# Kernel optimization log

Measured on AMD Instinct MI355X. Metric: run time of the kernel, lower is better.

## Reference

```python
import jax, jax.numpy as jnp
import numpy as np
import math

B, S, H, NH = 2, 2048, 2048, 16
HD = H // NH  # 128


def _rope_tables(seq_len, dim, base=10000.0):
    inv_freq = 1.0 / (base ** (np.arange(0, dim, 2, dtype=np.float32) / dim))
    t = np.arange(seq_len, dtype=np.float32)
    freqs = np.outer(t, inv_freq)                      # [S, dim/2]
    emb = np.concatenate([freqs, freqs], axis=-1)      # [S, dim] (HF layout)
    return jnp.asarray(np.cos(emb)), jnp.asarray(np.sin(emb))


def setup_inputs() -> dict:
    key = jax.random.key(0)
    ks = jax.random.split(key, 6)
    sc = 1.0 / math.sqrt(H)
    cos, sin = _rope_tables(S, HD)
    return {
        "hidden_states": jax.random.normal(ks[0], (B, S, H), jnp.float32),
        "wq": jax.random.normal(ks[1], (H, H), jnp.float32) * sc,
        "wk": jax.random.normal(ks[2], (H, H), jnp.float32) * sc,
        "wv": jax.random.normal(ks[3], (H, H), jnp.float32) * sc,
        "wo": jax.random.normal(ks[4], (H, H), jnp.float32) * sc,
        "cos": cos,
        "sin": sin,
        "attention_mask": jnp.ones((B, S), jnp.float32),
        "position_ids": jnp.broadcast_to(jnp.arange(S, dtype=jnp.int64), (B, S)),
    }


def _rotate_half(x):
    x1, x2 = jnp.split(x, 2, axis=-1)
    return jnp.concatenate([-x2, x1], axis=-1)


def reference(hidden_states, wq, wk, wv, wo, cos, sin, attention_mask, position_ids):
    b, s, _ = hidden_states.shape
    # projections (torch Linear: x @ W^T)
    q = (hidden_states @ wq.T).reshape(b, s, NH, HD).transpose(0, 2, 1, 3)
    k = (hidden_states @ wk.T).reshape(b, s, NH, HD).transpose(0, 2, 1, 3)
    v = (hidden_states @ wv.T).reshape(b, s, NH, HD).transpose(0, 2, 1, 3)
    # RoPE (HF apply_rotary_pos_emb): gather tables at position_ids -> [b,1,s,hd]
    c = cos[position_ids][:, None, :, :]
    sn = sin[position_ids][:, None, :, :]
    q = q * c + _rotate_half(q) * sn
    k = k * c + _rotate_half(k) * sn
    # dense attention scores [b,h,q,k]
    scores = jnp.einsum("bhqd,bhkd->bhqk", q, k) / math.sqrt(HD)
    adder = (1.0 - attention_mask)[:, None, None, :] * -10000.0
    scores = scores + adder
    probs = jax.nn.softmax(scores.astype(jnp.float32), axis=-1).astype(q.dtype)
    attn = jnp.einsum("bhqk,bhkd->bhqd", probs, v)
    attn = attn.transpose(0, 2, 1, 3).reshape(b, s, H)
    return attn @ wo.T
```

## Files before the change

### kernel.cpp

```cpp
#include <hip/hip_runtime.h>
#include <hip/hip_bf16.h>

#define B_SZ 2
#define S_LEN 2048
#define H_DIM 2048
#define N_HEAD 16
#define HD 128

using bf16 = __hip_bfloat16;
using bf16x8 = __bf16 __attribute__((ext_vector_type(8)));
using floatx4 = float __attribute__((ext_vector_type(4)));

typedef unsigned int __attribute__((address_space(1))) as1_uint;
typedef unsigned int __attribute__((address_space(3))) as3_uint;

__device__ inline void async_load16(const void* g, void* l) {
  __builtin_amdgcn_global_load_lds((const as1_uint*)g, (as3_uint*)l, 16, 0, 0);
}

__device__ inline void store_out(float* p, float v) { *p = v; }
__device__ inline void store_out(bf16* p, float v) { *p = __float2bfloat16(v); }

__global__ __launch_bounds__(256) void cast_kernel(const float* __restrict__ in,
                                                   bf16* __restrict__ out, int n4) {
  int i = blockIdx.x * 256 + threadIdx.x;
  if (i >= n4) return;
  const float4 v = ((const float4*)in)[i];
  union { bf16 h[4]; uint2 u; } o;
  o.h[0] = __float2bfloat16(v.x);
  o.h[1] = __float2bfloat16(v.y);
  o.h[2] = __float2bfloat16(v.z);
  o.h[3] = __float2bfloat16(v.w);
  ((uint2*)out)[i] = o.u;
}

__global__ __launch_bounds__(256) void cast4_kernel(
    const float* __restrict__ a, const float* __restrict__ b,
    const float* __restrict__ c, const float* __restrict__ d,
    bf16* __restrict__ oa, bf16* __restrict__ ob,
    bf16* __restrict__ oc, bf16* __restrict__ od) {
  int i = blockIdx.x * 256 + threadIdx.x;
  int sel = i >> 20;
  int j = i & 0xFFFFF;
  const float* src = sel == 0 ? a : sel == 1 ? b : sel == 2 ? c : d;
  bf16* dst = sel == 0 ? oa : sel == 1 ? ob : sel == 2 ? oc : od;
  const float4 v = ((const float4*)src)[j];
  union { bf16 h[4]; uint2 u; } o;
  o.h[0] = __float2bfloat16(v.x);
  o.h[1] = __float2bfloat16(v.y);
  o.h[2] = __float2bfloat16(v.z);
  o.h[3] = __float2bfloat16(v.w);
  ((uint2*)dst)[j] = o.u;
}

template <typename OutT>
__global__ __launch_bounds__(256) void gemm_bt(const bf16* __restrict__ A,
                                               const bf16* __restrict__ B,
                                               OutT* __restrict__ C,
                                               int M, int N, int K) {
  __shared__ alignas(16) bf16 As[128 * 32];
  __shared__ alignas(16) bf16 Bs[128 * 32];
  const int tid = threadIdx.x;
  const int wave = tid >> 6;
  const int lane = tid & 63;
  const int quad = lane >> 4;
  const int l16 = lane & 15;
  const int m0 = blockIdx.x * 128;
  const int n0 = blockIdx.y * 128;
  const int wm = (wave >> 1) * 64;
  const int wn = (wave & 1) * 64;

  const bf16* Ag = A + (size_t)(m0 + (tid >> 2)) * K + (tid & 3) * 8;
  const bf16* Bg = B + (size_t)(n0 + (tid >> 2)) * K + (tid & 3) * 8;
  char* AsB = (char*)As + wave * 1024;
  char* BsB = (char*)Bs + wave * 1024;
  const size_t rowskip = (size_t)64 * K;

  floatx4 acc[4][4] = {};

  for (int k0 = 0; k0 < K; k0 += 32) {
    async_load16(Ag + k0, AsB);
    async_load16(Ag + rowskip + k0, AsB + 4096);
    async_load16(Bg + k0, BsB);
    async_load16(Bg + rowskip + k0, BsB + 4096);
    __syncthreads();

    bf16x8 af[4], bfr[4];
#pragma unroll
    for (int i = 0; i < 4; i++)
      af[i] = *(const bf16x8*)&As[(wm + i * 16 + l16) * 32 + quad * 8];
#pragma unroll
    for (int j = 0; j < 4; j++)
      bfr[j] = *(const bf16x8*)&Bs[(wn + j * 16 + l16) * 32 + quad * 8];
#pragma unroll
    for (int i = 0; i < 4; i++)
#pragma unroll
      for (int j = 0; j < 4; j++)
        acc[i][j] = __builtin_amdgcn_mfma_f32_16x16x32_bf16(af[i], bfr[j], acc[i][j], 0, 0, 0);
    __syncthreads();
  }

#pragma unroll
  for (int i = 0; i < 4; i++) {
    const int row = m0 + wm + i * 16 + quad * 4;
#pragma unroll
    for (int j = 0; j < 4; j++) {
      const int col = n0 + wn + j * 16 + l16;
#pragma unroll
      for (int r = 0; r < 4; r++)
        store_out(&C[(size_t)(row + r) * N + col], acc[i][j][r]);
    }
  }
}

__global__ __launch_bounds__(256) void gemm_qk_rope(
    const bf16* __restrict__ A, const bf16* __restrict__ B, bf16* __restrict__ C,
    const float* __restrict__ cosT, const float* __restrict__ sinT,
    const int* __restrict__ pos, int K) {
  __shared__ alignas(16) bf16 As[128 * 32];
  __shared__ alignas(16) bf16 Bs[128 * 32];
  const int tid = threadIdx.x;
  const int wave = tid >> 6;
  const int lane = tid & 63;
  const int quad = lane >> 4;
  const int l16 = lane & 15;
  const int m0 = blockIdx.x * 128;
  const int n0 = blockIdx.y * 128;
  const int wm = wave * 32;

  const bf16* Ag = A + (size_t)(m0 + (tid >> 2)) * K + (tid & 3) * 8;
  const bf16* Bg = B + (size_t)(n0 + (tid >> 2)) * K + (tid & 3) * 8;
  char* AsB = (char*)As + wave * 1024;
  char* BsB = (char*)Bs + wave * 1024;
  const size_t rowskip = (size_t)64 * K;

  floatx4 acc[2][8] = {};

  for (int k0 = 0; k0 < K; k0 += 32) {
    async_load16(Ag + k0, AsB);
    async_load16(Ag + rowskip + k0, AsB + 4096);
    async_load16(Bg + k0, BsB);
    async_load16(Bg + rowskip + k0, BsB + 4096);
    __syncthreads();

    bf16x8 af[2], bfr[8];
#pragma unroll
    for (int i = 0; i < 2; i++)
      af[i] = *(const bf16x8*)&As[(wm + i * 16 + l16) * 32 + quad * 8];
#pragma unroll
    for (int j = 0; j < 8; j++)
      bfr[j] = *(const bf16x8*)&Bs[(j * 16 + l16) * 32 + quad * 8];
#pragma unroll
    for (int i = 0; i < 2; i++)
#pragma unroll
      for (int j = 0; j < 8; j++)
        acc[i][j] = __builtin_amdgcn_mfma_f32_16x16x32_bf16(af[i], bfr[j], acc[i][j], 0, 0, 0);
    __syncthreads();
  }

  const float sc = (n0 < 2048) ? 0.08838834764831845f : 1.0f;
#pragma unroll
  for (int i = 0; i < 2; i++) {
    const int row0 = m0 + wm + i * 16 + quad * 4;
#pragma unroll
    for (int r = 0; r < 4; r++) {
      const int row = row0 + r;
      const int p = pos[row];
      const float* cp = cosT + (size_t)p * HD;
      const float* sp = sinT + (size_t)p * HD;
      bf16* Crow = C + (size_t)row * 4096 + n0 + l16;
#pragma unroll
      for (int j = 0; j < 4; j++) {
        const int d = j * 16 + l16;
        const float c = cp[d], s = sp[d];
        const float v1 = acc[i][j][r], v2 = acc[i][j + 4][r];
        Crow[j * 16] = __float2bfloat16((v1 * c - v2 * s) * sc);
        Crow[j * 16 + 64] = __float2bfloat16((v2 * c + v1 * s) * sc);
      }
    }
  }
}

__global__ __launch_bounds__(256, 2) void flash_attn(
    const bf16* __restrict__ QK, const bf16* __restrict__ Vt,
    const float* __restrict__ mask, bf16* __restrict__ AO) {
  __shared__ alignas(16) bf16 KP[128 * 136];
  __shared__ alignas(16) bf16 Vs[128 * 136];
  const int tid = threadIdx.x;
  const int wave = tid >> 6;
  const int lane = tid & 63;
  const int quad = lane >> 4;
  const int l16 = lane & 15;
  const int b = blockIdx.x >> 4;
  const int h = blockIdx.x & 15;
  const int q0 = blockIdx.y * 128;

  const bf16* Qb = QK + (size_t)(b * S_LEN + q0) * 4096 + h * HD;
  const bf16* Kb = QK + (size_t)(b * S_LEN) * 4096 + 2048 + h * HD;
  const bf16* Vb = Vt + (size_t)(h * HD) * 4096 + (size_t)b * S_LEN;
  const float* Mb = mask + b * S_LEN;

  bf16x8 qf[2][4];
#pragma unroll
  for (int s = 0; s < 2; s++)
#pragma unroll
    for (int kc = 0; kc < 4; kc++)
      qf[s][kc] = *(const bf16x8*)(Qb + (size_t)(wave * 32 + s * 16 + l16) * 4096 +
                                   kc * 32 + quad * 8);

  float l_i[2][4] = {};
  floatx4 O[2][8] = {};

  for (int k0 = 0; k0 < S_LEN; k0 += 128) {
    for (int i = tid; i < 2048; i += 256) {
      int r = i >> 4;
      int c = (i & 15) * 8;
      *(uint4*)&KP[r * 136 + c] = *(const uint4*)(Kb + (size_t)(k0 + r) * 4096 + c);
      *(uint4*)&Vs[r * 136 + c] = *(const uint4*)(Vb + (size_t)r * 4096 + k0 + c);
    }
    __syncthreads();

    floatx4 Sa[2][8] = {};
#pragma unroll
    for (int ct = 0; ct < 8; ct++) {
      bf16x8 kf[4];
#pragma unroll
      for (int kc = 0; kc < 4; kc++)
        kf[kc] = *(const bf16x8*)&KP[(ct * 16 + l16) * 136 + kc * 32 + quad * 8];
#pragma unroll
      for (int s = 0; s < 2; s++)
#pragma unroll
        for (int kc = 0; kc < 4; kc++)
          Sa[s][ct] = __builtin_amdgcn_mfma_f32_16x16x32_bf16(qf[s][kc], kf[kc], Sa[s][ct], 0, 0, 0);
    }
    __syncthreads();

    float addv[8];
#pragma unroll
    for (int ct = 0; ct < 8; ct++)
      addv[ct] = (1.0f - Mb[k0 + ct * 16 + l16]) * -10000.0f - 12.0f;

#pragma unroll
    for (int s = 0; s < 2; s++) {
      const int qrow = (wave * 32 + s * 16 + quad * 4) * 136;
#pragma unroll
      for (int ct = 0; ct < 8; ct++)
#pragma unroll
        for (int r = 0; r < 4; r++) {
          float p = __expf(Sa[s][ct][r] + addv[ct]);
          l_i[s][r] += p;
          KP[qrow + r * 136 + ct * 16 + l16] = __float2bfloat16(p);
        }
    }

#pragma unroll
    for (int kc = 0; kc < 4; kc++) {
      bf16x8 pa[2];
#pragma unroll
      for (int s = 0; s < 2; s++)
        pa[s] = *(const bf16x8*)&KP[(wave * 32 + s * 16 + l16) * 136 + kc * 32 + quad * 8];
#pragma unroll
      for (int dt = 0; dt < 8; dt++) {
        bf16x8 vf = *(const bf16x8*)&Vs[(dt * 16 + l16) * 136 + kc * 32 + quad * 8];
#pragma unroll
        for (int s = 0; s < 2; s++)
          O[s][dt] = __builtin_amdgcn_mfma_f32_16x16x32_bf16(pa[s], vf, O[s][dt], 0, 0, 0);
      }
    }
    __syncthreads();
  }

#pragma unroll
  for (int s = 0; s < 2; s++)
#pragma unroll
    for (int r = 0; r < 4; r++)
#pragma unroll
      for (int off = 1; off < 16; off <<= 1)
        l_i[s][r] += __shfl_xor(l_i[s][r], off);

#pragma unroll
  for (int s = 0; s < 2; s++) {
    const int qrow = q0 + wave * 32 + s * 16 + quad * 4;
#pragma unroll
    for (int r = 0; r < 4; r++) {
      float inv = 1.0f / l_i[s][r];
      bf16* outp = AO + (size_t)(b * S_LEN + qrow + r) * H_DIM + h * HD + l16;
#pragma unroll
      for (int dt = 0; dt < 8; dt++)
        outp[dt * 16] = __float2bfloat16(O[s][dt][r] * inv);
    }
  }
}

extern "C" void kernel_launch(void* const* d_in, const int* in_sizes, int n_in,
                              void* d_out, int out_size, void* d_ws, size_t ws_size,
                              hipStream_t stream) {
  const float* hs   = (const float*)d_in[0];
  const float* wq   = (const float*)d_in[1];
  const float* wk   = (const float*)d_in[2];
  const float* wv   = (const float*)d_in[3];
  const float* wo   = (const float*)d_in[4];
  const float* cosT = (const float*)d_in[5];
  const float* sinT = (const float*)d_in[6];
  const float* mask = (const float*)d_in[7];
  const int*   pos  = (const int*)d_in[8];

  char* ws = (char*)d_ws;
  bf16* Xbf  = (bf16*)ws;
  bf16* Wqkb = (bf16*)(ws + (size_t)(16 << 20));
  bf16* Wvb  = (bf16*)(ws + (size_t)(32 << 20));
  bf16* Wob  = (bf16*)(ws + (size_t)(40 << 20));
  bf16* QKm  = (bf16*)(ws + (size_t)(48 << 20));
  bf16* Vtm  = (bf16*)(ws + (size_t)(80 << 20));
  bf16* AO   = Xbf;

  cast_kernel<<<8192, 256, 0, stream>>>(hs, Xbf, 2097152);
  cast4_kernel<<<16384, 256, 0, stream>>>(wq, wk, wv, wo,
                                          Wqkb, Wqkb + (size_t)2048 * 2048, Wvb, Wob);

  gemm_qk_rope<<<dim3(32, 32), 256, 0, stream>>>(Xbf, Wqkb, QKm, cosT, sinT, pos, 2048);
  gemm_bt<bf16><<<dim3(16, 32), 256, 0, stream>>>(Wvb, Xbf, Vtm, 2048, 4096, 2048);

  flash_attn<<<dim3(32, 16), 256, 0, stream>>>(QKm, Vtm, mask, AO);

  gemm_bt<float><<<dim3(32, 16), 256, 0, stream>>>(AO, Wob, (float*)d_out, 4096, 2048, 2048);
}
```

Measured before the change: 460.9 us.

## Rewrite QK+RoPE GEMM with 256x256 tiles and double-buffered swizzled LDS pipeline

```diff
diff --git a/kernel.cpp b/kernel.cpp
--- a/kernel.cpp
+++ b/kernel.cpp
@@ -113,64 +113,123 @@
   }
 }
 
-__global__ __launch_bounds__(256) void gemm_qk_rope(
-    const bf16* __restrict__ A, const bf16* __restrict__ B, bf16* __restrict__ C,
-    const float* __restrict__ cosT, const float* __restrict__ sinT,
-    const int* __restrict__ pos, int K) {
-  __shared__ alignas(16) bf16 As[128 * 32];
-  __shared__ alignas(16) bf16 Bs[128 * 32];
+__global__ __launch_bounds__(512, 2) void gemm_qk_rope256(
+    const bf16* __restrict__ A, const bf16* __restrict__ B,
+    bf16* __restrict__ C, const float* __restrict__ cosT,
+    const float* __restrict__ sinT, const int* __restrict__ pos) {
+  __shared__ alignas(16) char lds[131072];
   const int tid = threadIdx.x;
-  const int wave = tid >> 6;
+  const int wv = tid >> 6;
   const int lane = tid & 63;
   const int quad = lane >> 4;
   const int l16 = lane & 15;
-  const int m0 = blockIdx.x * 128;
-  const int n0 = blockIdx.y * 128;
-  const int wm = wave * 32;
-
-  const bf16* Ag = A + (size_t)(m0 + (tid >> 2)) * K + (tid & 3) * 8;
-  const bf16* Bg = B + (size_t)(n0 + (tid >> 2)) * K + (tid & 3) * 8;
-  char* AsB = (char*)As + wave * 1024;
-  char* BsB = (char*)Bs + wave * 1024;
-  const size_t rowskip = (size_t)64 * K;
-
-  floatx4 acc[2][8] = {};
-
-  for (int k0 = 0; k0 < K; k0 += 32) {
-    async_load16(Ag + k0, AsB);
-    async_load16(Ag + rowskip + k0, AsB + 4096);
-    async_load16(Bg + k0, BsB);
-    async_load16(Bg + rowskip + k0, BsB + 4096);
-    __syncthreads();
-
-    bf16x8 af[2], bfr[8];
-#pragma unroll
-    for (int i = 0; i < 2; i++)
-      af[i] = *(const bf16x8*)&As[(wm + i * 16 + l16) * 32 + quad * 8];
-#pragma unroll
-    for (int j = 0; j < 8; j++)
-      bfr[j] = *(const bf16x8*)&Bs[(j * 16 + l16) * 32 + quad * 8];
-#pragma unroll
-    for (int i = 0; i < 2; i++)
-#pragma unroll
-      for (int j = 0; j < 8; j++)
-        acc[i][j] = __builtin_amdgcn_mfma_f32_16x16x32_bf16(af[i], bfr[j], acc[i][j], 0, 0, 0);
-    __syncthreads();
-  }
-
-  const float sc = (n0 < 2048) ? 0.08838834764831845f : 1.0f;
-#pragma unroll
-  for (int i = 0; i < 2; i++) {
-    const int row0 = m0 + wm + i * 16 + quad * 4;
-#pragma unroll
-    for (int r = 0; r < 4; r++) {
-      const int row = row0 + r;
+  const int lrow = lane >> 3;
+  const int scol = ((lane & 7) << 4) ^ (lrow << 4);
+
+  const int id = blockIdx.x;
+  const int swz = (id & 7) * 32 + (id >> 3);
+  const int m0 = (swz >> 4) * 256;
+  const int n0 = (swz & 15) * 256;
+  const int wrow = (wv >> 1) * 64;
+  const int wcol = (wv & 1) * 128;
+
+  const char* Ag = (const char*)A + (size_t)(m0 + wv * 8 + lrow) * 4096 + scol;
+  const char* Bg = (const char*)B + (size_t)(n0 + wv * 8 + lrow) * 4096 + scol;
+  char* const ldsW = (char*)lds + wv * 1024;
+
+  const int csw0 = (quad << 4) ^ ((l16 & 7) << 4);
+  const int csw1 = csw0 ^ 64;
+
+  floatx4 acc[4][8] = {};
+  bf16x8 af[4][2], bfr[8][2];
+
+#define STAGE_A256(kt, buf) { \
+    const char* s_ = Ag + (size_t)(kt) * 128; \
+    char* d_ = ldsW + (buf) * 65536; \
+    async_load16(s_, d_); \
+    async_load16(s_ + (size_t)64 * 4096, d_ + 64 * 128); \
+    async_load16(s_ + (size_t)128 * 4096, d_ + 128 * 128); \
+    async_load16(s_ + (size_t)192 * 4096, d_ + 192 * 128); }
+#define STAGE_B256(kt, buf) { \
+    const char* s_ = Bg + (size_t)(kt) * 128; \
+    char* d_ = ldsW + (buf) * 65536 + 32768; \
+    async_load16(s_, d_); \
+    async_load16(s_ + (size_t)64 * 4096, d_ + 64 * 128); \
+    async_load16(s_ + (size_t)128 * 4096, d_ + 128 * 128); \
+    async_load16(s_ + (size_t)192 * 4096, d_ + 192 * 128); }
+#define READ_A256(I) { \
+    const char* p_ = cA + (wrow + (I) * 16 + l16) * 128; \
+    af[I][0] = *(const bf16x8*)(p_ + csw0); \
+    af[I][1] = *(const bf16x8*)(p_ + csw1); }
+#define READ_B256(J) { \
+    const char* p_ = cB + (wcol + (J) * 16 + l16) * 128; \
+    bfr[J][0] = *(const bf16x8*)(p_ + csw0); \
+    bfr[J][1] = *(const bf16x8*)(p_ + csw1); }
+#define MFMA_Q256(I0, J0) { \
+    _Pragma("unroll") for (int ks = 0; ks < 2; ++ks) \
+    _Pragma("unroll") for (int di = 0; di < 2; ++di) \
+    _Pragma("unroll") for (int dj = 0; dj < 4; ++dj) \
+      acc[(I0) + di][(J0) + dj] = __builtin_amdgcn_mfma_f32_16x16x32_bf16( \
+          af[(I0) + di][ks], bfr[(J0) + dj][ks], acc[(I0) + di][(J0) + dj], 0, 0, 0); }
+
+  STAGE_A256(0, 0) STAGE_B256(0, 0)
+  STAGE_A256(1, 1) STAGE_B256(1, 1)
+  asm volatile("s_waitcnt vmcnt(8)" ::: "memory");
+  __builtin_amdgcn_s_barrier();
+
+  const int NT = 32;
+  for (int t = 0; t < NT; ++t) {
+    const char* cA = (const char*)lds + (t & 1) * 65536;
+    const char* cB = cA + 32768;
+    READ_A256(0) READ_A256(1)
+    READ_B256(0) READ_B256(1) READ_B256(2) READ_B256(3)
+    __builtin_amdgcn_s_barrier();
+    asm volatile("s_waitcnt lgkmcnt(0)" ::: "memory");
+    __builtin_amdgcn_sched_barrier(0);
+    __builtin_amdgcn_s_setprio(1);
+    MFMA_Q256(0, 0)
+    __builtin_amdgcn_s_setprio(0);
+    __builtin_amdgcn_s_barrier();
+    READ_A256(2) READ_A256(3)
+    READ_B256(4) READ_B256(5) READ_B256(6) READ_B256(7)
+    __builtin_amdgcn_s_barrier();
+    asm volatile("s_waitcnt lgkmcnt(0)" ::: "memory");
+    __builtin_amdgcn_sched_barrier(0);
+    __builtin_amdgcn_s_setprio(1);
+    MFMA_Q256(2, 0)
+    __builtin_amdgcn_s_setprio(0);
+    __builtin_amdgcn_s_barrier();
+    __builtin_amdgcn_sched_barrier(0);
+    asm volatile("" ::: "memory");
+    if (t + 2 < NT) { STAGE_A256(t + 2, t & 1) }
+    __builtin_amdgcn_s_setprio(1);
+    MFMA_Q256(0, 4)
+    __builtin_amdgcn_s_setprio(0);
+    __builtin_amdgcn_s_barrier();
+    if (t + 2 < NT) { STAGE_B256(t + 2, t & 1) }
+    __builtin_amdgcn_s_setprio(1);
+    MFMA_Q256(2, 4)
+    __builtin_amdgcn_s_setprio(0);
+    if (t + 2 < NT) {
+      asm volatile("s_waitcnt vmcnt(8)" ::: "memory");
+    } else {
+      asm volatile("s_waitcnt vmcnt(0)" ::: "memory");
+    }
+    __builtin_amdgcn_s_barrier();
+  }
+
+  const float sc = ((n0 + wcol) < 2048) ? 0.08838834764831845f : 1.0f;
+#pragma unroll
+  for (int i = 0; i < 4; ++i) {
+#pragma unroll
+    for (int r = 0; r < 4; ++r) {
+      const int row = m0 + wrow + i * 16 + quad * 4 + r;
       const int p = pos[row];
       const float* cp = cosT + (size_t)p * HD;
       const float* sp = sinT + (size_t)p * HD;
-      bf16* Crow = C + (size_t)row * 4096 + n0 + l16;
-#pragma unroll
-      for (int j = 0; j < 4; j++) {
+      bf16* Crow = C + (size_t)row * 4096 + n0 + wcol + l16;
+#pragma unroll
+      for (int j = 0; j < 4; ++j) {
         const int d = j * 16 + l16;
         const float c = cp[d], s = sp[d];
         const float v1 = acc[i][j][r], v2 = acc[i][j + 4][r];
@@ -318,7 +377,7 @@
   cast4_kernel<<<16384, 256, 0, stream>>>(wq, wk, wv, wo,
                                           Wqkb, Wqkb + (size_t)2048 * 2048, Wvb, Wob);
 
-  gemm_qk_rope<<<dim3(32, 32), 256, 0, stream>>>(Xbf, Wqkb, QKm, cosT, sinT, pos, 2048);
+  gemm_qk_rope256<<<256, 512, 0, stream>>>(Xbf, Wqkb, QKm, cosT, sinT, pos);
   gemm_bt<bf16><<<dim3(16, 32), 256, 0, stream>>>(Wvb, Xbf, Vtm, 2048, 4096, 2048);
 
   flash_attn<<<dim3(32, 16), 256, 0, stream>>>(QKm, Vtm, mask, AO);
```

Result: faster. 428.3 us (-7.1%).
